# Performance work log

Hardware: AMD Instinct MI355X
Metric: run time of the kernel (lower is better)

Reference implementation:

```python
import jax, jax.numpy as jnp
import numpy as np

B, M, D, H, DH = 8, 1024, 768, 12, 64
R, RF, RW, DFF = 32, 384, 384, 3072
EPS = 1e-12  # BERT LayerNorm eps


def _ln(z, g, b):
    mu = jnp.mean(z, -1, keepdims=True)
    var = jnp.mean((z - mu) ** 2, -1, keepdims=True)
    return g * (z - mu) * jax.lax.rsqrt(var + EPS) + b


def setup_inputs() -> dict:
    ks = jax.random.split(jax.random.key(0), 20)
    n = lambda k, s: jax.random.normal(k, s, dtype=jnp.float32) * 0.02
    return {
        "x": jax.random.normal(ks[0], (B, M, D), dtype=jnp.float32),
        "mask": jnp.zeros((B, M), jnp.float32),  # additive attention mask
        "Pq": n(ks[1], (H, D, R)), "Vq": n(ks[2], (H, R, DH)), "bq": n(ks[3], (H, DH)),
        "Pk": n(ks[4], (H, D, R)), "Vk": n(ks[5], (H, R, DH)), "bk": n(ks[6], (H, DH)),
        "Pv": n(ks[7], (H, D, R)), "Vv": n(ks[8], (H, R, DH)), "bv": n(ks[9], (H, DH)),
        "Uo": n(ks[10], (D, RW)), "Vo": n(ks[11], (RW, D)), "bo_attn": n(ks[12], (D,)),
        "U1": n(ks[13], (D, RF)), "V1": n(ks[14], (RF, DFF)), "b1": n(ks[15], (DFF,)),
        "U2": n(ks[16], (DFF, RF)), "V2": n(ks[17], (RF, D)), "b2": n(ks[18], (D,)),
        "ln1_g": jnp.ones((D,), jnp.float32), "ln1_b": jnp.zeros((D,), jnp.float32),
        "ln2_g": jnp.ones((D,), jnp.float32), "ln2_b": jnp.zeros((D,), jnp.float32),
    }


def reference(x, mask, Pq, Vq, bq, Pk, Vk, bk, Pv, Vv, bv, Uo, Vo, bo_attn,
              U1, V1, b1, U2, V2, b2, ln1_g, ln1_b, ln2_g, ln2_b):
    Bx, Mx, dm = x.shape
    dh = dm // Pq.shape[0]
    scale = 1.0 / (dh ** 0.5)
    # low-rank per-head Q/K/V: x @ P (d->r) then @ V (r->dh), + per-head bias
    Q = jnp.einsum('bmd,hdr,hrk->bhmk', x, Pq, Vq) + bq[None, :, None, :]
    K = jnp.einsum('bmd,hdr,hrk->bhmk', x, Pk, Vk) + bk[None, :, None, :]
    V = jnp.einsum('bmd,hdr,hrk->bhmk', x, Pv, Vv) + bv[None, :, None, :]
    scores = jnp.einsum('bhmk,bhnk->bhmn', Q, K) * scale + mask[:, None, None, :]
    probs = jax.nn.softmax(scores, axis=-1)
    attn = jnp.einsum('bhmn,bhnk->bhmk', probs, V)
    attn = attn.transpose(0, 2, 1, 3).reshape(Bx, Mx, dm)  # (B, M, d_model)
    # low-rank attention output projection + residual + LN1
    x1 = _ln(x + (attn @ Uo) @ Vo + bo_attn, ln1_g, ln1_b)
    # low-rank FFN: GELU((x1 @ U1) @ V1 + b1) @ U2 @ V2 + b2 (BERT exact gelu)
    mid = x1 @ U1
    y = (jax.nn.gelu(mid @ V1 + b1, approximate=False) @ U2) @ V2 + b2
    return _ln(x1 + y, ln2_g, ln2_b)
```

## Files before the change

### kernel.cpp

```cpp
#include <hip/hip_runtime.h>
#include <cstddef>

#define D_MODEL 768
#define NHEAD   12
#define DHEAD   64
#define RANK    32
#define SEQ     1024
#define BATCH   8
#define BM      8192

typedef __attribute__((ext_vector_type(8))) short short8;
typedef __attribute__((ext_vector_type(4))) float floatx4;

__device__ inline ushort f2b(float f) {
  union { float f; unsigned u; } v; v.f = f;
  unsigned r = v.u + 0x7fffu + ((v.u >> 16) & 1u);
  return (ushort)(r >> 16);
}
__device__ inline float b2f(ushort h) {
  union { unsigned u; float f; } v; v.u = ((unsigned)h) << 16;
  return v.f;
}
__device__ inline unsigned pk2(float a, float b) {
  return ((__float_as_uint(b) + 0x8000u) & 0xffff0000u) |
         ((__float_as_uint(a) + 0x8000u) >> 16);
}
__device__ inline float fast_gelu(float x) {
  float z = 0.79788456080286536f * (x + 0.044715f * x * x * x);
  float e = __expf(2.f * z);
  float t = 1.f - 2.f / (e + 1.f);
  return 0.5f * x * (1.f + t);
}

__global__ __launch_bounds__(256) void f2b_kernel(
    const float* __restrict__ in, ushort* __restrict__ out, int n) {
  int i = (blockIdx.x * 256 + threadIdx.x) * 4;
  if (i >= n) return;
  float4 v = *(const float4*)(in + i);
  ushort4 o;
  o.x = f2b(v.x); o.y = f2b(v.y); o.z = f2b(v.z); o.w = f2b(v.w);
  *(ushort4*)(out + i) = o;
}

__global__ __launch_bounds__(256) void combine_qkv_kernel(
    const float* __restrict__ Pq, const float* __restrict__ Vq,
    const float* __restrict__ Pk, const float* __restrict__ Vk,
    const float* __restrict__ Pv, const float* __restrict__ Vv,
    ushort* __restrict__ Wt) {
  int which = blockIdx.y;
  const float* P  = which == 0 ? Pq : (which == 1 ? Pk : Pv);
  const float* Vw = which == 0 ? Vq : (which == 1 ? Vk : Vv);
  ushort* W = Wt + (size_t)which * D_MODEL * D_MODEL;
  int idx = blockIdx.x * 256 + threadIdx.x;
  if (idx >= D_MODEL * NHEAD * DHEAD) return;
  int c = idx / D_MODEL;
  int d = idx - c * D_MODEL;
  int h = c >> 6, k = c & 63;
  const float* p = P + ((size_t)h * D_MODEL + d) * RANK;
  const float* v = Vw + (size_t)h * RANK * DHEAD + k;
  float s = 0.f;
#pragma unroll
  for (int r = 0; r < RANK; r++) s += p[r] * v[(size_t)r * DHEAD];
  W[(size_t)c * D_MODEL + d] = f2b(s);
}

__global__ __launch_bounds__(256) void concat_bias_kernel(
    const float* __restrict__ bq, const float* __restrict__ bk,
    const float* __restrict__ bv, float* __restrict__ out) {
  int i = blockIdx.x * 256 + threadIdx.x;
  if (i >= 2304) return;
  out[i] = (i < 768) ? bq[i] : (i < 1536 ? bk[i - 768] : bv[i - 1536]);
}

__global__ __launch_bounds__(256) void prep_weights_kernel(
    const float* __restrict__ U1, const float* __restrict__ V1,
    const float* __restrict__ U2, const float* __restrict__ V2,
    const float* __restrict__ Vo, const float* __restrict__ Uo,
    ushort* __restrict__ U1t, ushort* __restrict__ V1t,
    ushort* __restrict__ U2t, ushort* __restrict__ V2t,
    ushort* __restrict__ VoT, ushort* __restrict__ Uob) {
  __shared__ float t[32][33];
  int blk = blockIdx.x;
  if (blk >= 3168) {
    int i = (blk - 3168) * 1024 + threadIdx.x * 4;
    float4 v = *(const float4*)(Uo + i);
    ushort4 o;
    o.x = f2b(v.x); o.y = f2b(v.y); o.z = f2b(v.z); o.w = f2b(v.w);
    *(ushort4*)(Uob + i) = o;
    return;
  }
  const float* in; ushort* out; int R, C, bx, by;
  if (blk < 288)       { in = U1; out = U1t; R = 768;  C = 384;  int i = blk;        bx = i % 12; by = i / 12; }
  else if (blk < 1440) { in = V1; out = V1t; R = 384;  C = 3072; int i = blk - 288;  bx = i % 96; by = i / 96; }
  else if (blk < 2592) { in = U2; out = U2t; R = 3072; C = 384;  int i = blk - 1440; bx = i % 12; by = i / 12; }
  else if (blk < 2880) { in = V2; out = V2t; R = 384;  C = 768;  int i = blk - 2592; bx = i % 24; by = i / 24; }
  else                 { in = Vo; out = VoT; R = 384;  C = 768;  int i = blk - 2880; bx = i % 24; by = i / 24; }
  int c0 = bx * 32, r0 = by * 32;
  int lx = threadIdx.x & 31, ly = threadIdx.x >> 5;
#pragma unroll
  for (int i = 0; i < 32; i += 8)
    t[ly + i][lx] = in[(size_t)(r0 + ly + i) * C + c0 + lx];
  __syncthreads();
#pragma unroll
  for (int i = 0; i < 32; i += 8)
    out[(size_t)(c0 + ly + i) * R + r0 + lx] = f2b(t[lx][ly + i]);
}

template <int OUTMODE, int BIAS, int GELU>
__global__ __launch_bounds__(256, 2) void gemm_mfma_kernel(
    const ushort* __restrict__ A, const ushort* __restrict__ Bt,
    const float* __restrict__ bias, void* __restrict__ C,
    void* __restrict__ C2, void* __restrict__ C3,
    int M, int N, int K) {
  __shared__ __align__(16) ushort Als[2][128 * 64];
  __shared__ __align__(16) ushort Bls[2][128 * 64];
  const int tid  = threadIdx.x;
  const int lane = tid & 63;
  const int quad = lane >> 4, l16 = lane & 15;
  const int wu   = __builtin_amdgcn_readfirstlane(tid >> 6);
  const int wrow = (wu >> 1) * 64, wcol = (wu & 1) * 64;
  const int row0 = blockIdx.x * 128, col0 = blockIdx.y * 128;

  const int r_ = tid >> 3, sl_ = tid & 7;
  const ushort* Ag = A + (size_t)(row0 + r_) * K + sl_ * 8;
  const ushort* Bg = Bt + (size_t)(col0 + r_) * K + sl_ * 8;
  const int loff = r_ * 64 + ((sl_ ^ (r_ & 7)) << 3);

  const int nsteps = K >> 6;
  short8 ast[4], bst[4];

#pragma unroll
  for (int p = 0; p < 4; p++) {
    ast[p] = *(const short8*)(Ag + (size_t)(32 * p) * K);
    bst[p] = *(const short8*)(Bg + (size_t)(32 * p) * K);
  }
#pragma unroll
  for (int p = 0; p < 4; p++) {
    *(short8*)(&Als[0][0] + loff + p * (32 * 64)) = ast[p];
    *(short8*)(&Bls[0][0] + loff + p * (32 * 64)) = bst[p];
  }
#pragma unroll
  for (int p = 0; p < 4; p++) {
    ast[p] = *(const short8*)(Ag + (size_t)(32 * p) * K + 64);
    bst[p] = *(const short8*)(Bg + (size_t)(32 * p) * K + 64);
  }
  asm volatile("s_waitcnt lgkmcnt(0)" ::: "memory");
  __builtin_amdgcn_s_barrier();
  asm volatile("" ::: "memory");

  floatx4 acc[4][4] = {};

  for (int s = 0; s < nsteps; s++) {
    const int cur = s & 1;

    if (s + 1 < nsteps) {
#pragma unroll
      for (int p = 0; p < 4; p++) {
        *(short8*)(&Als[cur ^ 1][0] + loff + p * (32 * 64)) = ast[p];
        *(short8*)(&Bls[cur ^ 1][0] + loff + p * (32 * 64)) = bst[p];
      }
      if (s + 2 < nsteps) {
        const int ko = (s + 2) * 64;
#pragma unroll
        for (int p = 0; p < 4; p++) {
          ast[p] = *(const short8*)(Ag + (size_t)(32 * p) * K + ko);
          bst[p] = *(const short8*)(Bg + (size_t)(32 * p) * K + ko);
        }
      }
    }

    __builtin_amdgcn_s_setprio(1);
#pragma unroll
    for (int kk = 0; kk < 2; kk++) {
      short8 af[4], bf[4];
#pragma unroll
      for (int mt = 0; mt < 4; mt++) {
        int row = wrow + mt * 16 + l16;
        af[mt] = *(const short8*)(&Als[cur][0] + row * 64
                                  + (((kk * 4 + quad) ^ (l16 & 7)) << 3));
      }
#pragma unroll
      for (int nt = 0; nt < 4; nt++) {
        int row = wcol + nt * 16 + l16;
        bf[nt] = *(const short8*)(&Bls[cur][0] + row * 64
                                  + (((kk * 4 + quad) ^ (l16 & 7)) << 3));
      }
#pragma unroll
      for (int mt = 0; mt < 4; mt++)
#pragma unroll
        for (int nt = 0; nt < 4; nt++)
          acc[mt][nt] = __builtin_amdgcn_mfma_f32_16x16x32_bf16(
              af[mt], bf[nt], acc[mt][nt], 0, 0, 0);
    }
    __builtin_amdgcn_s_setprio(0);

    if (s + 1 < nsteps) {
      asm volatile("s_waitcnt lgkmcnt(0)" ::: "memory");
      __builtin_amdgcn_s_barrier();
      asm volatile("" ::: "memory");
    }
  }

#pragma unroll
  for (int mt = 0; mt < 4; mt++) {
#pragma unroll
    for (int nt = 0; nt < 4; nt++) {
      int colg = col0 + wcol + nt * 16 + l16;
      float bv_ = BIAS ? bias[colg] : 0.f;
      float v4[4];
#pragma unroll
      for (int r = 0; r < 4; r++) {
        float v = acc[mt][nt][r] + bv_;
        if (GELU) v = fast_gelu(v);
        v4[r] = v;
      }
      int rowg0 = row0 + wrow + mt * 16 + quad * 4;
      if (OUTMODE == 3) {
        int seg = col0 / 768;
        int cl = colg - seg * 768;
        if (seg == 2) {
          ushort4 o;
          o.x = f2b(v4[0]); o.y = f2b(v4[1]); o.z = f2b(v4[2]); o.w = f2b(v4[3]);
          *(ushort4*)((ushort*)C3 + (size_t)cl * BM + rowg0) = o;
        } else {
          ushort* dst = (seg == 0) ? (ushort*)C : (ushort*)C2;
          float sc = (seg == 0) ? 0.125f : 1.f;
#pragma unroll
          for (int r = 0; r < 4; r++)
            dst[(size_t)(rowg0 + r) * D_MODEL + cl] = f2b(v4[r] * sc);
        }
      } else {
#pragma unroll
        for (int r = 0; r < 4; r++)
          ((ushort*)C)[(size_t)(rowg0 + r) * N + colg] = f2b(v4[r]);
      }
    }
  }
}

__global__ __launch_bounds__(256, 2) void gemm_piped_splitk_kernel(
    const ushort* __restrict__ A, const ushort* __restrict__ Bt,
    float* __restrict__ Cpart, int M, int N, int Ktot, int Kper) {
  __shared__ __align__(16) ushort Als[2][128 * 64];
  __shared__ __align__(16) ushort Bls[2][128 * 64];
  const int tid  = threadIdx.x;
  const int lane = tid & 63;
  const int quad = lane >> 4, l16 = lane & 15;
  const int wu   = __builtin_amdgcn_readfirstlane(tid >> 6);
  const int wrow = (wu >> 1) * 64, wcol = (wu & 1) * 64;
  const int row0 = blockIdx.x * 128, col0 = blockIdx.y * 128;
  const int kbase = blockIdx.z * Kper;
  float* Cz = Cpart + (size_t)blockIdx.z * M * N;

  const int r_ = tid >> 3, sl_ = tid & 7;
  const ushort* Ag = A + (size_t)(row0 + r_) * Ktot + kbase + sl_ * 8;
  const ushort* Bg = Bt + (size_t)(col0 + r_) * Ktot + kbase + sl_ * 8;
  const int loff = r_ * 64 + ((sl_ ^ (r_ & 7)) << 3);

  const int nsteps = Kper >> 6;
  short8 ast[4], bst[4];

#pragma unroll
  for (int p = 0; p < 4; p++) {
    ast[p] = *(const short8*)(Ag + (size_t)(32 * p) * Ktot);
    bst[p] = *(const short8*)(Bg + (size_t)(32 * p) * Ktot);
  }
#pragma unroll
  for (int p = 0; p < 4; p++) {
    *(short8*)(&Als[0][0] + loff + p * (32 * 64)) = ast[p];
    *(short8*)(&Bls[0][0] + loff + p * (32 * 64)) = bst[p];
  }
#pragma unroll
  for (int p = 0; p < 4; p++) {
    ast[p] = *(const short8*)(Ag + (size_t)(32 * p) * Ktot + 64);
    bst[p] = *(const short8*)(Bg + (size_t)(32 * p) * Ktot + 64);
  }
  asm volatile("s_waitcnt lgkmcnt(0)" ::: "memory");
  __builtin_amdgcn_s_barrier();
  asm volatile("" ::: "memory");

  floatx4 acc[4][4] = {};

  for (int s = 0; s < nsteps; s++) {
    const int cur = s & 1;

    if (s + 1 < nsteps) {
#pragma unroll
      for (int p = 0; p < 4; p++) {
        *(short8*)(&Als[cur ^ 1][0] + loff + p * (32 * 64)) = ast[p];
        *(short8*)(&Bls[cur ^ 1][0] + loff + p * (32 * 64)) = bst[p];
      }
      if (s + 2 < nsteps) {
        const int ko = (s + 2) * 64;
#pragma unroll
        for (int p = 0; p < 4; p++) {
          ast[p] = *(const short8*)(Ag + (size_t)(32 * p) * Ktot + ko);
          bst[p] = *(const short8*)(Bg + (size_t)(32 * p) * Ktot + ko);
        }
      }
    }

    __builtin_amdgcn_s_setprio(1);
#pragma unroll
    for (int kk = 0; kk < 2; kk++) {
      short8 af[4], bf[4];
#pragma unroll
      for (int mt = 0; mt < 4; mt++) {
        int row = wrow + mt * 16 + l16;
        af[mt] = *(const short8*)(&Als[cur][0] + row * 64
                                  + (((kk * 4 + quad) ^ (l16 & 7)) << 3));
      }
#pragma unroll
      for (int nt = 0; nt < 4; nt++) {
        int row = wcol + nt * 16 + l16;
        bf[nt] = *(const short8*)(&Bls[cur][0] + row * 64
                                  + (((kk * 4 + quad) ^ (l16 & 7)) << 3));
      }
#pragma unroll
      for (int mt = 0; mt < 4; mt++)
#pragma unroll
        for (int nt = 0; nt < 4; nt++)
          acc[mt][nt] = __builtin_amdgcn_mfma_f32_16x16x32_bf16(
              af[mt], bf[nt], acc[mt][nt], 0, 0, 0);
    }
    __builtin_amdgcn_s_setprio(0);

    if (s + 1 < nsteps) {
      asm volatile("s_waitcnt lgkmcnt(0)" ::: "memory");
      __builtin_amdgcn_s_barrier();
      asm volatile("" ::: "memory");
    }
  }

#pragma unroll
  for (int mt = 0; mt < 4; mt++)
#pragma unroll
    for (int nt = 0; nt < 4; nt++) {
      int colg = col0 + wcol + nt * 16 + l16;
      int rowg0 = row0 + wrow + mt * 16 + quad * 4;
#pragma unroll
      for (int r = 0; r < 4; r++)
        Cz[(size_t)(rowg0 + r) * N + colg] = acc[mt][nt][r];
    }
}

__global__ __launch_bounds__(256) void reduce_splitk_kernel(
    const float* __restrict__ part, ushort* __restrict__ out, int n, int S) {
  int i = (blockIdx.x * 256 + threadIdx.x) * 4;
  if (i >= n) return;
  float4 a = *(const float4*)(part + i);
  for (int s = 1; s < S; s++) {
    float4 b = *(const float4*)(part + (size_t)s * n + i);
    a.x += b.x; a.y += b.y; a.z += b.z; a.w += b.w;
  }
  ushort4 o;
  o.x = f2b(a.x); o.y = f2b(a.y); o.z = f2b(a.z); o.w = f2b(a.w);
  *(ushort4*)(out + i) = o;
}

template <int BIAS>
__global__ __launch_bounds__(256) void gemm_n64_kernel(
    const ushort* __restrict__ A, const ushort* __restrict__ Bt,
    const float* __restrict__ bias, ushort* __restrict__ C,
    int M, int N, int K) {
  __shared__ __align__(16) ushort Als[128 * 32];
  __shared__ __align__(16) ushort Bls[64 * 32];
  const int tid  = threadIdx.x;
  const int lane = tid & 63;
  const int quad = lane >> 4, l16 = lane & 15;
  const int wu   = __builtin_amdgcn_readfirstlane(tid >> 6);
  const int row0 = blockIdx.x * 128, col0 = blockIdx.y * 64;

  floatx4 acc[2][4] = {};

  for (int k0 = 0; k0 < K; k0 += 32) {
    __syncthreads();
#pragma unroll
    for (int is = 0; is < 2; is++) {
      int c = is * 256 + wu * 64 + lane;
      int m = c >> 2, kk = (c & 3) << 3;
      const ushort* ga = A + (size_t)(row0 + m) * K + (k0 + kk);
      ushort* la = Als + (size_t)(is * 256 + wu * 64) * 8;
      __builtin_amdgcn_global_load_lds(
          (const __attribute__((address_space(1))) void*)ga,
          (__attribute__((address_space(3))) void*)la, 16, 0, 0);
    }
    {
      int c = wu * 64 + lane;
      int m = c >> 2, kk = (c & 3) << 3;
      const ushort* gb = Bt + (size_t)(col0 + m) * K + (k0 + kk);
      ushort* lb = Bls + (size_t)(wu * 64) * 8;
      __builtin_amdgcn_global_load_lds(
          (const __attribute__((address_space(1))) void*)gb,
          (__attribute__((address_space(3))) void*)lb, 16, 0, 0);
    }
    __syncthreads();

    short8 af[2], bf[4];
#pragma unroll
    for (int mt = 0; mt < 2; mt++)
      af[mt] = *(const short8*)(Als + ((wu * 32 + mt * 16 + l16) * 32 + quad * 8));
#pragma unroll
    for (int nt = 0; nt < 4; nt++)
      bf[nt] = *(const short8*)(Bls + ((nt * 16 + l16) * 32 + quad * 8));
#pragma unroll
    for (int mt = 0; mt < 2; mt++)
#pragma unroll
      for (int nt = 0; nt < 4; nt++)
        acc[mt][nt] = __builtin_amdgcn_mfma_f32_16x16x32_bf16(
            af[mt], bf[nt], acc[mt][nt], 0, 0, 0);
  }

#pragma unroll
  for (int mt = 0; mt < 2; mt++) {
#pragma unroll
    for (int nt = 0; nt < 4; nt++) {
      int colg = col0 + nt * 16 + l16;
      float bv_ = BIAS ? bias[colg] : 0.f;
      int rowg0 = row0 + wu * 32 + mt * 16 + quad * 4;
#pragma unroll
      for (int r = 0; r < 4; r++)
        C[(size_t)(rowg0 + r) * N + colg] = f2b(acc[mt][nt][r] + bv_);
    }
  }
}

__global__ __launch_bounds__(256, 3) void attn_mfma_kernel(
    const ushort* __restrict__ Q, const ushort* __restrict__ K,
    const ushort* __restrict__ Vt, const float* __restrict__ mask,
    ushort* __restrict__ O) {
  const int bid  = blockIdx.x;
  const int xcd  = bid & 7;
  const int rest = bid >> 3;
  const int qt   = rest & 7;
  const int grp  = (rest >> 3) * 8 + xcd;
  const int h = grp % 12, b = grp / 12;

  const int tid = threadIdx.x;
  const int lane = tid & 63;
  const int quad = lane >> 4, l16 = lane & 15;
  const int wu = __builtin_amdgcn_readfirstlane(tid >> 6);
  const int qrow0 = qt * 128 + wu * 32;

  __shared__ __align__(16) ushort Ks[2][64 * 64];
  __shared__ __align__(16) ushort Vts[2][64 * 64];
  __shared__ __align__(16) float Msk[SEQ];

  *(float4*)(Msk + tid * 4) = *(const float4*)(mask + (size_t)b * SEQ + tid * 4);

  short8 qf[2][2];
#pragma unroll
  for (int rt = 0; rt < 2; rt++) {
    const ushort* qp = Q + ((size_t)(b * SEQ + qrow0 + rt * 16 + l16)) * D_MODEL
                     + h * DHEAD + quad * 8;
    qf[rt][0] = *(const short8*)qp;
    qf[rt][1] = *(const short8*)(qp + 32);
  }

  const int j0 = tid >> 3, ck = tid & 7;
  const ushort* Kg = K + ((size_t)(b * SEQ + j0)) * D_MODEL + h * DHEAD + ck * 8;
  const ushort* Vg = Vt + ((size_t)(h * DHEAD + j0)) * BM + b * SEQ + ck * 8;
  const int kloff = j0 * 64 + ((ck ^ (j0 & 7)) << 3);

  short8 kst[2], vst[2];
#pragma unroll
  for (int p = 0; p < 2; p++) {
    kst[p] = *(const short8*)(Kg + (size_t)(p * 32) * D_MODEL);
    vst[p] = *(const short8*)(Vg + (size_t)p * (32 * BM));
  }
#pragma unroll
  for (int p = 0; p < 2; p++) {
    *(short8*)(&Ks[0][0] + kloff + p * (32 * 64)) = kst[p];
    *(short8*)(&Vts[0][0] + kloff + p * (32 * 64)) = vst[p];
  }
#pragma unroll
  for (int p = 0; p < 2; p++) {
    kst[p] = *(const short8*)(Kg + (size_t)(64 + p * 32) * D_MODEL);
    vst[p] = *(const short8*)(Vg + 64 + (size_t)p * (32 * BM));
  }
  asm volatile("s_waitcnt lgkmcnt(0)" ::: "memory");
  __builtin_amdgcn_s_barrier();
  asm volatile("" ::: "memory");

  float lsum[2] = {0.f, 0.f};
  floatx4 o_acc[2][4] = {};

  for (int n0 = 0; n0 < SEQ; n0 += 64) {
    const int cur = (n0 >> 6) & 1;

    if (n0 + 64 < SEQ) {
#pragma unroll
      for (int p = 0; p < 2; p++) {
        *(short8*)(&Ks[cur ^ 1][0] + kloff + p * (32 * 64)) = kst[p];
        *(short8*)(&Vts[cur ^ 1][0] + kloff + p * (32 * 64)) = vst[p];
      }
      if (n0 + 128 < SEQ) {
#pragma unroll
        for (int p = 0; p < 2; p++) {
          kst[p] = *(const short8*)(Kg + (size_t)(n0 + 128 + p * 32) * D_MODEL);
          vst[p] = *(const short8*)(Vg + (n0 + 128) + (size_t)p * (32 * BM));
        }
      }
    }

    __builtin_amdgcn_s_setprio(1);
    unsigned UA[2][4], UB[2][4];
#pragma unroll
    for (int ct = 0; ct < 4; ct++) {
      int krow = ct * 16 + l16;
      int sa = (quad ^ (l16 & 7)) << 3;
      const ushort* kbp = &Ks[cur][0] + krow * 64;
      short8 ka = *(const short8*)(kbp + sa);
      short8 kb = *(const short8*)(kbp + (sa ^ 32));
      float4 mk = *(const float4*)(Msk + n0 + ct * 16 + quad * 4);
#pragma unroll
      for (int rt = 0; rt < 2; rt++) {
        floatx4 st = {};
        st = __builtin_amdgcn_mfma_f32_16x16x32_bf16(ka, qf[rt][0], st, 0, 0, 0);
        st = __builtin_amdgcn_mfma_f32_16x16x32_bf16(kb, qf[rt][1], st, 0, 0, 0);
        float e0 = __expf(st[0] + mk.x);
        float e1 = __expf(st[1] + mk.y);
        float e2 = __expf(st[2] + mk.z);
        float e3 = __expf(st[3] + mk.w);
        lsum[rt] += (e0 + e1) + (e2 + e3);
        UA[rt][ct] = pk2(e0, e1);
        UB[rt][ct] = pk2(e2, e3);
      }
    }

#pragma unroll
    for (int kk = 0; kk < 2; kk++) {
      short8 pa[2];
#pragma unroll
      for (int rt = 0; rt < 2; rt++) {
        unsigned a0 = UA[rt][2 * kk], a2 = UA[rt][2 * kk + 1];
        unsigned b1 = UB[rt][2 * kk], b3 = UB[rt][2 * kk + 1];
        asm("v_permlane32_swap_b32 %0, %1" : "+v"(a0), "+v"(a2));
        asm("v_permlane16_swap_b32 %0, %1" : "+v"(a0), "+v"(a2));
        asm("v_permlane32_swap_b32 %0, %1" : "+v"(b1), "+v"(b3));
        asm("v_permlane16_swap_b32 %0, %1" : "+v"(b1), "+v"(b3));
        int4 t;
        t.x = (int)a0;
        t.y = (int)b1;
        t.z = (int)a2;
        t.w = (int)b3;
        pa[rt] = *(short8*)&t;
      }
#pragma unroll
      for (int dt = 0; dt < 4; dt++) {
        int vr = dt * 16 + l16;
        short8 vb = *(const short8*)(&Vts[cur][0] + vr * 64
                                     + (((kk * 4 + quad) ^ (l16 & 7)) << 3));
#pragma unroll
        for (int rt = 0; rt < 2; rt++)
          o_acc[rt][dt] = __builtin_amdgcn_mfma_f32_16x16x32_bf16(
              pa[rt], vb, o_acc[rt][dt], 0, 0, 0);
      }
    }
    __builtin_amdgcn_s_setprio(0);

    if (n0 + 64 < SEQ) {
      asm volatile("s_waitcnt lgkmcnt(0)" ::: "memory");
      __builtin_amdgcn_s_barrier();
      asm volatile("" ::: "memory");
    }
  }

#pragma unroll
  for (int rt = 0; rt < 2; rt++) {
    float l = lsum[rt];
    l += __shfl_xor(l, 16);
    l += __shfl_xor(l, 32);
    float inv = 1.f / l;
    int lanebase = lane & 48;
#pragma unroll
    for (int rr = 0; rr < 4; rr++) {
      int iv = __builtin_amdgcn_ds_bpermute((lanebase | (quad * 4 + rr)) << 2,
                                            __float_as_int(inv));
      float invr = __int_as_float(iv);
      size_t rowg = (size_t)(b * SEQ + qrow0 + rt * 16 + quad * 4 + rr);
#pragma unroll
      for (int dt = 0; dt < 4; dt++)
        O[rowg * D_MODEL + h * DHEAD + dt * 16 + l16] = f2b(o_acc[rt][dt][rr] * invr);
    }
  }
}

template <int AIN_BF16, int OUT_FP32, int OUT_BF16>
__global__ __launch_bounds__(256) void add_ln_kernel(
    const float* __restrict__ Ainf, const ushort* __restrict__ Ainb,
    const ushort* __restrict__ Binb,
    const float* __restrict__ g, const float* __restrict__ bt,
    float* __restrict__ outf, ushort* __restrict__ outb) {
  const int row = blockIdx.x, tid = threadIdx.x;
  __shared__ float red[4];
  float v[3];
  float s = 0.f;
#pragma unroll
  for (int u = 0; u < 3; u++) {
    int c = tid + u * 256;
    float a = AIN_BF16 ? b2f(Ainb[(size_t)row * 768 + c]) : Ainf[(size_t)row * 768 + c];
    v[u] = a + b2f(Binb[(size_t)row * 768 + c]);
    s += v[u];
  }
#pragma unroll
  for (int off = 32; off > 0; off >>= 1) s += __shfl_down(s, off);
  if ((tid & 63) == 0) red[tid >> 6] = s;
  __syncthreads();
  float mu = (red[0] + red[1] + red[2] + red[3]) * (1.f / 768.f);
  float s2 = 0.f;
#pragma unroll
  for (int u = 0; u < 3; u++) { float d = v[u] - mu; s2 += d * d; }
#pragma unroll
  for (int off = 32; off > 0; off >>= 1) s2 += __shfl_down(s2, off);
  __syncthreads();
  if ((tid & 63) == 0) red[tid >> 6] = s2;
  __syncthreads();
  float var = (red[0] + red[1] + red[2] + red[3]) * (1.f / 768.f);
  float inv = rsqrtf(var + 1e-12f);
#pragma unroll
  for (int u = 0; u < 3; u++) {
    int c = tid + u * 256;
    float r = g[c] * (v[u] - mu) * inv + bt[c];
    if (OUT_FP32) outf[(size_t)row * 768 + c] = r;
    if (OUT_BF16) outb[(size_t)row * 768 + c] = f2b(r);
  }
}

extern "C" void kernel_launch(void* const* d_in, const int* in_sizes, int n_in,
                              void* d_out, int out_size, void* d_ws, size_t ws_size,
                              hipStream_t stream) {
  const float* x    = (const float*)d_in[0];
  const float* mask = (const float*)d_in[1];
  const float* Pq   = (const float*)d_in[2];
  const float* Vq   = (const float*)d_in[3];
  const float* bq   = (const float*)d_in[4];
  const float* Pk   = (const float*)d_in[5];
  const float* Vk   = (const float*)d_in[6];
  const float* bk   = (const float*)d_in[7];
  const float* Pv   = (const float*)d_in[8];
  const float* Vv   = (const float*)d_in[9];
  const float* bv   = (const float*)d_in[10];
  const float* Uo   = (const float*)d_in[11];
  const float* Vo   = (const float*)d_in[12];
  const float* bo   = (const float*)d_in[13];
  const float* U1   = (const float*)d_in[14];
  const float* V1   = (const float*)d_in[15];
  const float* b1   = (const float*)d_in[16];
  const float* U2   = (const float*)d_in[17];
  const float* V2   = (const float*)d_in[18];
  const float* b2   = (const float*)d_in[19];
  const float* g1   = (const float*)d_in[20];
  const float* be1  = (const float*)d_in[21];
  const float* g2   = (const float*)d_in[22];
  const float* be2  = (const float*)d_in[23];

  char* w = (char*)d_ws;
  auto alloc = [&](size_t bytes) -> char* {
    char* p = w; w += (bytes + 255) & ~(size_t)255; return p;
  };
  ushort* xb     = (ushort*)alloc((size_t)BM * 768 * 2);
  ushort* Wqkvt  = (ushort*)alloc((size_t)2304 * 768 * 2);
  float*  ball   = (float*)alloc(2304 * 4);
  ushort* VoT    = (ushort*)alloc(768 * 384 * 2);
  ushort* Uob    = (ushort*)alloc(768 * 384 * 2);
  ushort* Wot    = (ushort*)alloc(768 * 768 * 2);
  ushort* U1t    = (ushort*)alloc(384 * 768 * 2);
  ushort* V1t    = (ushort*)alloc((size_t)3072 * 384 * 2);
  ushort* U2t    = (ushort*)alloc((size_t)384 * 3072 * 2);
  ushort* V2t    = (ushort*)alloc(768 * 384 * 2);
  ushort* Qb     = (ushort*)alloc((size_t)BM * 768 * 2);
  ushort* Kb     = (ushort*)alloc((size_t)BM * 768 * 2);
  ushort* Vtb    = (ushort*)alloc((size_t)768 * BM * 2);
  ushort* attnb  = (ushort*)alloc((size_t)BM * 768 * 2);
  ushort* mtb    = (ushort*)alloc((size_t)BM * 384 * 2);
  ushort* y1b    = (ushort*)alloc((size_t)BM * 768 * 2);
  ushort* x1b    = (ushort*)alloc((size_t)BM * 768 * 2);
  float*  part   = (float*)alloc((size_t)4 * BM * 384 * 4);
  ushort* hiddenb = Qb;
  ushort* y2b     = y1b;
  float*  outp    = (float*)d_out;

  f2b_kernel<<<(BM * 768) / 1024, 256, 0, stream>>>(x, xb, BM * 768);
  combine_qkv_kernel<<<dim3(2304, 3), 256, 0, stream>>>(Pq, Vq, Pk, Vk, Pv, Vv, Wqkvt);
  concat_bias_kernel<<<9, 256, 0, stream>>>(bq, bk, bv, ball);
  prep_weights_kernel<<<3456, 256, 0, stream>>>(U1, V1, U2, V2, Vo, Uo,
                                                U1t, V1t, U2t, V2t, VoT, Uob);
  gemm_n64_kernel<0><<<dim3(6, 12), 256, 0, stream>>>(VoT, Uob, nullptr, Wot, 768, 768, 384);

  gemm_mfma_kernel<3, 1, 0><<<dim3(64, 18), 256, 0, stream>>>(
      xb, Wqkvt, ball, Qb, Kb, Vtb, BM, 2304, 768);

  attn_mfma_kernel<<<dim3(768), 256, 0, stream>>>(Qb, Kb, Vtb, mask, attnb);

  gemm_mfma_kernel<1, 1, 0><<<dim3(64, 6), 256, 0, stream>>>(
      attnb, Wot, bo, y1b, nullptr, nullptr, BM, 768, 768);
  add_ln_kernel<0, 0, 1><<<BM, 256, 0, stream>>>(x, nullptr, y1b, g1, be1, nullptr, x1b);

  gemm_mfma_kernel<1, 0, 0><<<dim3(64, 3), 256, 0, stream>>>(
      x1b, U1t, nullptr, mtb, nullptr, nullptr, BM, 384, 768);
  gemm_mfma_kernel<1, 1, 1><<<dim3(64, 24), 256, 0, stream>>>(
      mtb, V1t, b1, hiddenb, nullptr, nullptr, BM, 3072, 384);
  gemm_piped_splitk_kernel<<<dim3(64, 3, 2), 256, 0, stream>>>(
      hiddenb, U2t, part, BM, 384, 3072, 1536);
  reduce_splitk_kernel<<<(BM * 384) / 1024, 256, 0, stream>>>(part, mtb, BM * 384, 2);
  gemm_mfma_kernel<1, 1, 0><<<dim3(64, 6), 256, 0, stream>>>(
      mtb, V2t, b2, y2b, nullptr, nullptr, BM, 768, 384);

  add_ln_kernel<1, 1, 0><<<BM, 256, 0, stream>>>(nullptr, x1b, y2b, g2, be2, outp, nullptr);
}
```

Measured before the change: 388.3 us.

## Add double-buffered 128x64 GEMM for narrow projections; one-wave-per-row LayerNorm

Adds a register-staged, double-buffered LDS GEMM kernel with 128x64 tiles that replaces the generic MFMA GEMM for the attention output, U1 and V2 projections. The grid doubles in the N dimension and more blocks fit per CU, aiming at better occupancy and overlap of global loads with MFMA on these small-N GEMMs. Separately, the add+LayerNorm kernel now processes one row per wavefront using xor-shuffle reductions, removing shared-memory reductions and block barriers. The trade-off is less reuse of the A operand per block (A tiles are reloaded twice as often) and more registers per thread in LayerNorm.

Result: no change. 380.9 us (-1.9%).

```diff
diff --git a/kernel.cpp b/kernel.cpp
--- a/kernel.cpp
+++ b/kernel.cpp
@@ -238,6 +238,121 @@
   }
 }
 
+template <int BIAS, int GELU>
+__global__ __launch_bounds__(256, 3) void gemm_piped_n64_kernel(
+    const ushort* __restrict__ A, const ushort* __restrict__ Bt,
+    const float* __restrict__ bias, ushort* __restrict__ C,
+    int M, int N, int K) {
+  __shared__ __align__(16) ushort Als[2][128 * 64];
+  __shared__ __align__(16) ushort Bls[2][64 * 64];
+  const int tid  = threadIdx.x;
+  const int lane = tid & 63;
+  const int quad = lane >> 4, l16 = lane & 15;
+  const int wu   = __builtin_amdgcn_readfirstlane(tid >> 6);
+  const int row0 = blockIdx.x * 128, col0 = blockIdx.y * 64;
+
+  const int r_ = tid >> 3, sl_ = tid & 7;
+  const ushort* Ag = A + (size_t)(row0 + r_) * K + sl_ * 8;
+  const ushort* Bg = Bt + (size_t)(col0 + r_) * K + sl_ * 8;
+  const int loff = r_ * 64 + ((sl_ ^ (r_ & 7)) << 3);
+
+  const int nsteps = K >> 6;
+  short8 ast[4], bst[2];
+
+#pragma unroll
+  for (int p = 0; p < 4; p++)
+    ast[p] = *(const short8*)(Ag + (size_t)(32 * p) * K);
+#pragma unroll
+  for (int p = 0; p < 2; p++)
+    bst[p] = *(const short8*)(Bg + (size_t)(32 * p) * K);
+#pragma unroll
+  for (int p = 0; p < 4; p++)
+    *(short8*)(&Als[0][0] + loff + p * (32 * 64)) = ast[p];
+#pragma unroll
+  for (int p = 0; p < 2; p++)
+    *(short8*)(&Bls[0][0] + loff + p * (32 * 64)) = bst[p];
+#pragma unroll
+  for (int p = 0; p < 4; p++)
+    ast[p] = *(const short8*)(Ag + (size_t)(32 * p) * K + 64);
+#pragma unroll
+  for (int p = 0; p < 2; p++)
+    bst[p] = *(const short8*)(Bg + (size_t)(32 * p) * K + 64);
+  asm volatile("s_waitcnt lgkmcnt(0)" ::: "memory");
+  __builtin_amdgcn_s_barrier();
+  asm volatile("" ::: "memory");
+
+  floatx4 acc[2][4] = {};
+
+  for (int s = 0; s < nsteps; s++) {
+    const int cur = s & 1;
+
+    if (s + 1 < nsteps) {
+#pragma unroll
+      for (int p = 0; p < 4; p++)
+        *(short8*)(&Als[cur ^ 1][0] + loff + p * (32 * 64)) = ast[p];
+#pragma unroll
+      for (int p = 0; p < 2; p++)
+        *(short8*)(&Bls[cur ^ 1][0] + loff + p * (32 * 64)) = bst[p];
+      if (s + 2 < nsteps) {
+        const int ko = (s + 2) * 64;
+#pragma unroll
+        for (int p = 0; p < 4; p++)
+          ast[p] = *(const short8*)(Ag + (size_t)(32 * p) * K + ko);
+#pragma unroll
+        for (int p = 0; p < 2; p++)
+          bst[p] = *(const short8*)(Bg + (size_t)(32 * p) * K + ko);
+      }
+    }
+
+    __builtin_amdgcn_s_setprio(1);
+#pragma unroll
+    for (int kk = 0; kk < 2; kk++) {
+      short8 af[2], bf[4];
+#pragma unroll
+      for (int mt = 0; mt < 2; mt++) {
+        int row = wu * 32 + mt * 16 + l16;
+        af[mt] = *(const short8*)(&Als[cur][0] + row * 64
+                                  + (((kk * 4 + quad) ^ (l16 & 7)) << 3));
+      }
+#pragma unroll
+      for (int nt = 0; nt < 4; nt++) {
+        int row = nt * 16 + l16;
+        bf[nt] = *(const short8*)(&Bls[cur][0] + row * 64
+                                  + (((kk * 4 + quad) ^ (l16 & 7)) << 3));
+      }
+#pragma unroll
+      for (int mt = 0; mt < 2; mt++)
+#pragma unroll
+        for (int nt = 0; nt < 4; nt++)
+          acc[mt][nt] = __builtin_amdgcn_mfma_f32_16x16x32_bf16(
+              af[mt], bf[nt], acc[mt][nt], 0, 0, 0);
+    }
+    __builtin_amdgcn_s_setprio(0);
+
+    if (s + 1 < nsteps) {
+      asm volatile("s_waitcnt lgkmcnt(0)" ::: "memory");
+      __builtin_amdgcn_s_barrier();
+      asm volatile("" ::: "memory");
+    }
+  }
+
+#pragma unroll
+  for (int mt = 0; mt < 2; mt++) {
+#pragma unroll
+    for (int nt = 0; nt < 4; nt++) {
+      int colg = col0 + nt * 16 + l16;
+      float bv_ = BIAS ? bias[colg] : 0.f;
+      int rowg0 = row0 + wu * 32 + mt * 16 + quad * 4;
+#pragma unroll
+      for (int r = 0; r < 4; r++) {
+        float v = acc[mt][nt][r] + bv_;
+        if (GELU) v = fast_gelu(v);
+        C[(size_t)(rowg0 + r) * N + colg] = f2b(v);
+      }
+    }
+  }
+}
+
 __global__ __launch_bounds__(256, 2) void gemm_piped_splitk_kernel(
     const ushort* __restrict__ A, const ushort* __restrict__ Bt,
     float* __restrict__ Cpart, int M, int N, int Ktot, int Kper) {
@@ -592,38 +707,33 @@
     const ushort* __restrict__ Binb,
     const float* __restrict__ g, const float* __restrict__ bt,
     float* __restrict__ outf, ushort* __restrict__ outb) {
-  const int row = blockIdx.x, tid = threadIdx.x;
-  __shared__ float red[4];
-  float v[3];
+  const int lane = threadIdx.x & 63;
+  const int row  = blockIdx.x * 4 + (threadIdx.x >> 6);
+  const size_t base = (size_t)row * 768;
+  float v[12];
   float s = 0.f;
 #pragma unroll
-  for (int u = 0; u < 3; u++) {
-    int c = tid + u * 256;
-    float a = AIN_BF16 ? b2f(Ainb[(size_t)row * 768 + c]) : Ainf[(size_t)row * 768 + c];
-    v[u] = a + b2f(Binb[(size_t)row * 768 + c]);
+  for (int u = 0; u < 12; u++) {
+    int c = lane + u * 64;
+    float a = AIN_BF16 ? b2f(Ainb[base + c]) : Ainf[base + c];
+    v[u] = a + b2f(Binb[base + c]);
     s += v[u];
   }
 #pragma unroll
-  for (int off = 32; off > 0; off >>= 1) s += __shfl_down(s, off);
-  if ((tid & 63) == 0) red[tid >> 6] = s;
-  __syncthreads();
-  float mu = (red[0] + red[1] + red[2] + red[3]) * (1.f / 768.f);
+  for (int off = 32; off > 0; off >>= 1) s += __shfl_xor(s, off);
+  float mu = s * (1.f / 768.f);
   float s2 = 0.f;
 #pragma unroll
-  for (int u = 0; u < 3; u++) { float d = v[u] - mu; s2 += d * d; }
-#pragma unroll
-  for (int off = 32; off > 0; off >>= 1) s2 += __shfl_down(s2, off);
-  __syncthreads();
-  if ((tid & 63) == 0) red[tid >> 6] = s2;
-  __syncthreads();
-  float var = (red[0] + red[1] + red[2] + red[3]) * (1.f / 768.f);
-  float inv = rsqrtf(var + 1e-12f);
-#pragma unroll
-  for (int u = 0; u < 3; u++) {
-    int c = tid + u * 256;
+  for (int u = 0; u < 12; u++) { float d = v[u] - mu; s2 += d * d; }
+#pragma unroll
+  for (int off = 32; off > 0; off >>= 1) s2 += __shfl_xor(s2, off);
+  float inv = rsqrtf(s2 * (1.f / 768.f) + 1e-12f);
+#pragma unroll
+  for (int u = 0; u < 12; u++) {
+    int c = lane + u * 64;
     float r = g[c] * (v[u] - mu) * inv + bt[c];
-    if (OUT_FP32) outf[(size_t)row * 768 + c] = r;
-    if (OUT_BF16) outb[(size_t)row * 768 + c] = f2b(r);
+    if (OUT_FP32) outf[base + c] = r;
+    if (OUT_BF16) outb[base + c] = f2b(r);
   }
 }
 
@@ -693,19 +803,19 @@
 
   attn_mfma_kernel<<<dim3(768), 256, 0, stream>>>(Qb, Kb, Vtb, mask, attnb);
 
-  gemm_mfma_kernel<1, 1, 0><<<dim3(64, 6), 256, 0, stream>>>(
-      attnb, Wot, bo, y1b, nullptr, nullptr, BM, 768, 768);
-  add_ln_kernel<0, 0, 1><<<BM, 256, 0, stream>>>(x, nullptr, y1b, g1, be1, nullptr, x1b);
-
-  gemm_mfma_kernel<1, 0, 0><<<dim3(64, 3), 256, 0, stream>>>(
-      x1b, U1t, nullptr, mtb, nullptr, nullptr, BM, 384, 768);
+  gemm_piped_n64_kernel<1, 0><<<dim3(64, 12), 256, 0, stream>>>(
+      attnb, Wot, bo, y1b, BM, 768, 768);
+  add_ln_kernel<0, 0, 1><<<BM / 4, 256, 0, stream>>>(x, nullptr, y1b, g1, be1, nullptr, x1b);
+
+  gemm_piped_n64_kernel<0, 0><<<dim3(64, 6), 256, 0, stream>>>(
+      x1b, U1t, nullptr, mtb, BM, 384, 768);
   gemm_mfma_kernel<1, 1, 1><<<dim3(64, 24), 256, 0, stream>>>(
       mtb, V1t, b1, hiddenb, nullptr, nullptr, BM, 3072, 384);
   gemm_piped_splitk_kernel<<<dim3(64, 3, 2), 256, 0, stream>>>(
       hiddenb, U2t, part, BM, 384, 3072, 1536);
   reduce_splitk_kernel<<<(BM * 384) / 1024, 256, 0, stream>>>(part, mtb, BM * 384, 2);
-  gemm_mfma_kernel<1, 1, 0><<<dim3(64, 6), 256, 0, stream>>>(
-      mtb, V2t, b2, y2b, nullptr, nullptr, BM, 768, 384);
-
-  add_ln_kernel<1, 1, 0><<<BM, 256, 0, stream>>>(nullptr, x1b, y2b, g2, be2, outp, nullptr);
-}
+  gemm_piped_n64_kernel<1, 0><<<dim3(64, 12), 256, 0, stream>>>(
+      mtb, V2t, b2, y2b, BM, 768, 384);
+
+  add_ln_kernel<1, 1, 0><<<BM / 4, 256, 0, stream>>>(nullptr, x1b, y2b, g2, be2, outp, nullptr);
+}
```
